# Performance work log

Hardware: AMD Instinct MI355X
Metric: run time of the kernel (lower is better)

Reference implementation:

```python
import jax, jax.numpy as jnp
import numpy as np

IMG_SIZE = 224  # matches init_kwargs img_size


def setup_inputs() -> dict:
    key = jax.random.key(0)
    k1, k2, k3 = jax.random.split(key, 3)
    B, N = 128, 16384
    points = jax.random.uniform(k1, (B, N, 3), dtype=jnp.float32, minval=-1.0, maxval=1.0)
    azimuth = jax.random.uniform(k2, (B,), dtype=jnp.float32, minval=0.0, maxval=2.0 * np.pi)
    elevation = jax.random.uniform(k3, (B,), dtype=jnp.float32, minval=-0.5, maxval=0.5)
    return {"points": points, "azimuth": azimuth, "elevation": elevation}


def _rotation_matrices(azimuth, elevation):
    cა, sა = jnp.cos(azimuth), jnp.sin(azimuth)
    ce, se = jnp.cos(elevation), jnp.sin(elevation)
    z = jnp.zeros_like(cა)
    o = jnp.ones_like(cა)
    # R_az: rotation about y-axis, shape (B,3,3)
    R_az = jnp.stack([
        jnp.stack([cა, z, sა], -1),
        jnp.stack([z, o, z], -1),
        jnp.stack([-sა, z, cა], -1),
    ], axis=-2)
    # R_el: rotation about x-axis
    R_el = jnp.stack([
        jnp.stack([o, z, z], -1),
        jnp.stack([z, ce, -se], -1),
        jnp.stack([z, se, ce], -1),
    ], axis=-2)
    return jnp.einsum('bij,bjk->bik', R_el, R_az)


def reference(points, azimuth, elevation):
    B, N, _ = points.shape
    H = W = IMG_SIZE
    R = _rotation_matrices(azimuth, elevation)                 # (B,3,3)
    rotated = jnp.einsum('bni,bji->bnj', points, R)            # points @ R^T -> (B,N,3)

    points_2d = rotated[..., :2]
    z = rotated[..., 2]
    z_min = jnp.min(z, axis=1, keepdims=True)
    z_max = jnp.max(z, axis=1, keepdims=True)
    feat = 0.3 + 0.7 * (z - z_min) / (z_max - z_min + 1e-6)    # (B,N)

    px = (points_2d[..., 0] + 1.0) * 0.5 * W - 0.5
    py = (points_2d[..., 1] + 1.0) * 0.5 * H - 0.5
    px1 = jnp.floor(px); py1 = jnp.floor(py)
    px2 = px1 + 1.0;     py2 = py1 + 1.0

    w11 = (px2 - px) * (py2 - py)
    w12 = (px2 - px) * (py - py1)
    w21 = (px - px1) * (py2 - py)
    w22 = (px - px1) * (py - py1)

    mask = (px1 >= 0) & (py1 >= 0) & (px2 < W) & (py2 < H)     # (B,N)
    # fuse mask + feature into the weights instead of compacting (jit-friendly)
    vals = jnp.stack([w11, w12, w21, w22], axis=-1)            # (B,N,4)
    vals = vals * (feat * mask.astype(feat.dtype))[..., None]

    px1i = jnp.clip(px1, 0, W - 1).astype(jnp.int32)
    py1i = jnp.clip(py1, 0, H - 1).astype(jnp.int32)
    px2i = jnp.clip(px2, 0, W - 1).astype(jnp.int32)
    py2i = jnp.clip(py2, 0, H - 1).astype(jnp.int32)
    base = (jnp.arange(B, dtype=jnp.int32) * (H * W))[:, None]  # (B,1)
    idx = jnp.stack([
        base + py1i * W + px1i,
        base + py2i * W + px1i,
        base + py1i * W + px2i,
        base + py2i * W + px2i,
    ], axis=-1)                                                 # (B,N,4)

    image = jnp.zeros(B * H * W, dtype=vals.dtype)
    image = image.at[idx.reshape(-1)].add(vals.reshape(-1))
    image = image.reshape(B, 1, H, W)
    return jnp.broadcast_to(image, (B, 3, H, W))
```

## Files before the change

kernel.cpp:

```cpp
#include <hip/hip_runtime.h>

#define IMG 224
#define HW (IMG * IMG)
#define HW4 (HW / 4)
#define NB 128
#define NPTS 16384

#define QUARTERS 4
#define RPB (IMG / QUARTERS)
#define TILE_FLOATS (RPB * IMG)
#define THREADS 512

__global__ __launch_bounds__(THREADS) void k_render(const float* __restrict__ pts,
                                                    const float* __restrict__ az,
                                                    const float* __restrict__ el,
                                                    float* __restrict__ out) {
    const int b = blockIdx.x & (NB - 1);
    const int q = blockIdx.x >> 7;
    const int y0 = q * RPB;

    __shared__ float tile[TILE_FLOATS];
    __shared__ float wmin[THREADS / 64], wmax[THREADS / 64];

    float sa, ca, se, ce;
    __sincosf(az[b], &sa, &ca);
    __sincosf(el[b], &se, &ce);
    const float r00 = ca,       r02 = sa;
    const float r10 = se * sa,  r11 = ce,  r12 = -se * ca;
    const float r20 = -ce * sa, r21 = se,  r22 = ce * ca;

    for (int i = threadIdx.x; i < TILE_FLOATS; i += THREADS) tile[i] = 0.0f;

    const float4* __restrict__ pb4 = (const float4*)(pts + (size_t)b * NPTS * 3);

    float zmin = 1e30f, zmax = -1e30f;
    for (int it = 0; it < NPTS / (4 * THREADS); ++it) {
        const int t = it * THREADS + threadIdx.x;
        const float4 v0 = pb4[3 * t + 0];
        const float4 v1 = pb4[3 * t + 1];
        const float4 v2 = pb4[3 * t + 2];
        float rz;
        rz = r20 * v0.x + r21 * v0.y + r22 * v0.z; zmin = fminf(zmin, rz); zmax = fmaxf(zmax, rz);
        rz = r20 * v0.w + r21 * v1.x + r22 * v1.y; zmin = fminf(zmin, rz); zmax = fmaxf(zmax, rz);
        rz = r20 * v1.z + r21 * v1.w + r22 * v2.x; zmin = fminf(zmin, rz); zmax = fmaxf(zmax, rz);
        rz = r20 * v2.y + r21 * v2.z + r22 * v2.w; zmin = fminf(zmin, rz); zmax = fmaxf(zmax, rz);
    }
    for (int m = 1; m < 64; m <<= 1) {
        zmin = fminf(zmin, __shfl_xor(zmin, m));
        zmax = fmaxf(zmax, __shfl_xor(zmax, m));
    }
    const int wid = threadIdx.x >> 6;
    if ((threadIdx.x & 63) == 0) { wmin[wid] = zmin; wmax[wid] = zmax; }
    __syncthreads();
    zmin = wmin[0]; zmax = wmax[0];
#pragma unroll
    for (int w = 1; w < THREADS / 64; ++w) {
        zmin = fminf(zmin, wmin[w]);
        zmax = fmaxf(zmax, wmax[w]);
    }
    const float inv = 0.7f / (zmax - zmin + 1e-6f);

    auto splat = [&](float x, float y, float z) {
        const float rx = r00 * x + r02 * z;
        const float ry = r10 * x + r11 * y + r12 * z;
        const float rz = r20 * x + r21 * y + r22 * z;
        const float feat = 0.3f + (rz - zmin) * inv;

        const float px = (rx + 1.0f) * (0.5f * IMG) - 0.5f;
        const float py = (ry + 1.0f) * (0.5f * IMG) - 0.5f;
        const float px1 = floorf(px);
        const float py1 = floorf(py);
        if (px1 >= 0.0f && py1 >= 0.0f && px1 < (float)(IMG - 1) && py1 < (float)(IMG - 1)) {
            const float wx2 = px - px1;
            const float wx1 = 1.0f - wx2;
            const float wy2 = py - py1;
            const float wy1 = 1.0f - wy2;

            const int ix = (int)px1;
            const int iy = (int)py1;
            const int r0 = iy - y0;
            const int r1 = r0 + 1;
            if (r0 >= 0 && r0 < RPB) {
                atomicAdd(&tile[r0 * IMG + ix],     wx1 * wy1 * feat);
                atomicAdd(&tile[r0 * IMG + ix + 1], wx2 * wy1 * feat);
            }
            if (r1 >= 0 && r1 < RPB) {
                atomicAdd(&tile[r1 * IMG + ix],     wx1 * wy2 * feat);
                atomicAdd(&tile[r1 * IMG + ix + 1], wx2 * wy2 * feat);
            }
        }
    };

    for (int it = 0; it < NPTS / (4 * THREADS); ++it) {
        const int t = it * THREADS + threadIdx.x;
        const float4 v0 = pb4[3 * t + 0];
        const float4 v1 = pb4[3 * t + 1];
        const float4 v2 = pb4[3 * t + 2];
        splat(v0.x, v0.y, v0.z);
        splat(v0.w, v1.x, v1.y);
        splat(v1.z, v1.w, v2.x);
        splat(v2.y, v2.z, v2.w);
    }

    __syncthreads();

    const float4* __restrict__ t4 = (const float4*)tile;
    float4* __restrict__ o4 = (float4*)(out + (size_t)b * 3 * HW + (size_t)y0 * IMG);
    for (int i = threadIdx.x; i < TILE_FLOATS / 4; i += THREADS) {
        const float4 v = t4[i];
        o4[i] = v;
        o4[i + HW4] = v;
        o4[i + 2 * HW4] = v;
    }
}

extern "C" void kernel_launch(void* const* d_in, const int* in_sizes, int n_in,
                              void* d_out, int out_size, void* d_ws, size_t ws_size,
                              hipStream_t stream) {
    const float* pts = (const float*)d_in[0];
    const float* az  = (const float*)d_in[1];
    const float* el  = (const float*)d_in[2];
    float* out = (float*)d_out;

    k_render<<<NB * QUARTERS, THREADS, 0, stream>>>(pts, az, el, out);
}
```

Before: 133.5 us.

## Split render into transform/min-max prep kernel and row-banded splat kernel

After: 148.0 us. 10.8% more time.

```diff
diff --git a/kernel.cpp b/kernel.cpp
--- a/kernel.cpp
+++ b/kernel.cpp
@@ -6,21 +6,26 @@
 #define NB 128
 #define NPTS 16384
 
-#define QUARTERS 4
-#define RPB (IMG / QUARTERS)
-#define TILE_FLOATS (RPB * IMG)
-#define THREADS 512
+#define PACKED_FLOATS ((size_t)NB * NPTS * 3)
+#define MINKEY_BYTE_OFF (PACKED_FLOATS * sizeof(float))
 
-__global__ __launch_bounds__(THREADS) void k_render(const float* __restrict__ pts,
-                                                    const float* __restrict__ az,
-                                                    const float* __restrict__ el,
-                                                    float* __restrict__ out) {
+__device__ __forceinline__ unsigned fkey(float f) {
+    unsigned u = __float_as_uint(f);
+    return (u & 0x80000000u) ? ~u : (u | 0x80000000u);
+}
+__device__ __forceinline__ float fdec(unsigned k) {
+    unsigned u = (k & 0x80000000u) ? (k & 0x7FFFFFFFu) : ~k;
+    return __uint_as_float(u);
+}
+
+__global__ __launch_bounds__(256) void k_prep(const float* __restrict__ pts,
+                                              const float* __restrict__ az,
+                                              const float* __restrict__ el,
+                                              float* __restrict__ packed,
+                                              unsigned* __restrict__ minkeys,
+                                              unsigned* __restrict__ maxkeys) {
     const int b = blockIdx.x & (NB - 1);
-    const int q = blockIdx.x >> 7;
-    const int y0 = q * RPB;
-
-    __shared__ float tile[TILE_FLOATS];
-    __shared__ float wmin[THREADS / 64], wmax[THREADS / 64];
+    const int chunk = blockIdx.x >> 7;
 
     float sa, ca, se, ce;
     __sincosf(az[b], &sa, &ca);
@@ -29,53 +34,85 @@
     const float r10 = se * sa,  r11 = ce,  r12 = -se * ca;
     const float r20 = -ce * sa, r21 = se,  r22 = ce * ca;
 
-    for (int i = threadIdx.x; i < TILE_FLOATS; i += THREADS) tile[i] = 0.0f;
-
     const float4* __restrict__ pb4 = (const float4*)(pts + (size_t)b * NPTS * 3);
+    float4* __restrict__ pk4 = (float4*)(packed + (size_t)b * NPTS * 3);
 
     float zmin = 1e30f, zmax = -1e30f;
-    for (int it = 0; it < NPTS / (4 * THREADS); ++it) {
-        const int t = it * THREADS + threadIdx.x;
+
+    auto xform = [&](float x, float y, float z, float& px, float& py, float& rz) {
+        const float rx = r00 * x + r02 * z;
+        const float ry = r10 * x + r11 * y + r12 * z;
+        rz = r20 * x + r21 * y + r22 * z;
+        px = (rx + 1.0f) * (0.5f * IMG) - 0.5f;
+        py = (ry + 1.0f) * (0.5f * IMG) - 0.5f;
+        zmin = fminf(zmin, rz);
+        zmax = fmaxf(zmax, rz);
+    };
+
+#pragma unroll
+    for (int it = 0; it < 2; ++it) {
+        const int t = chunk * 512 + it * 256 + threadIdx.x;
         const float4 v0 = pb4[3 * t + 0];
         const float4 v1 = pb4[3 * t + 1];
         const float4 v2 = pb4[3 * t + 2];
-        float rz;
-        rz = r20 * v0.x + r21 * v0.y + r22 * v0.z; zmin = fminf(zmin, rz); zmax = fmaxf(zmax, rz);
-        rz = r20 * v0.w + r21 * v1.x + r22 * v1.y; zmin = fminf(zmin, rz); zmax = fmaxf(zmax, rz);
-        rz = r20 * v1.z + r21 * v1.w + r22 * v2.x; zmin = fminf(zmin, rz); zmax = fmaxf(zmax, rz);
-        rz = r20 * v2.y + r21 * v2.z + r22 * v2.w; zmin = fminf(zmin, rz); zmax = fmaxf(zmax, rz);
+        float px0, py0, rz0, px1, py1, rz1, px2, py2, rz2, px3, py3, rz3;
+        xform(v0.x, v0.y, v0.z, px0, py0, rz0);
+        xform(v0.w, v1.x, v1.y, px1, py1, rz1);
+        xform(v1.z, v1.w, v2.x, px2, py2, rz2);
+        xform(v2.y, v2.z, v2.w, px3, py3, rz3);
+        pk4[3 * t + 0] = make_float4(px0, py0, rz0, px1);
+        pk4[3 * t + 1] = make_float4(py1, rz1, px2, py2);
+        pk4[3 * t + 2] = make_float4(rz2, px3, py3, rz3);
     }
+
     for (int m = 1; m < 64; m <<= 1) {
         zmin = fminf(zmin, __shfl_xor(zmin, m));
         zmax = fmaxf(zmax, __shfl_xor(zmax, m));
     }
+    __shared__ float wmin[4], wmax[4];
     const int wid = threadIdx.x >> 6;
     if ((threadIdx.x & 63) == 0) { wmin[wid] = zmin; wmax[wid] = zmax; }
     __syncthreads();
-    zmin = wmin[0]; zmax = wmax[0];
-#pragma unroll
-    for (int w = 1; w < THREADS / 64; ++w) {
-        zmin = fminf(zmin, wmin[w]);
-        zmax = fmaxf(zmax, wmax[w]);
+    if (threadIdx.x == 0) {
+        zmin = fminf(fminf(wmin[0], wmin[1]), fminf(wmin[2], wmin[3]));
+        zmax = fmaxf(fmaxf(wmax[0], wmax[1]), fmaxf(wmax[2], wmax[3]));
+        atomicMin(&minkeys[b], fkey(zmin));
+        atomicMax(&maxkeys[b], fkey(zmax));
     }
+}
+
+#define GROUPS 8
+#define RPB (IMG / GROUPS)
+#define TILE_FLOATS (RPB * IMG)
+#define BTHREADS 512
+
+__global__ __launch_bounds__(BTHREADS) void k_splat(const float* __restrict__ packed,
+                                                    const unsigned* __restrict__ minkeys,
+                                                    const unsigned* __restrict__ maxkeys,
+                                                    float* __restrict__ out) {
+    const int b = blockIdx.x & (NB - 1);
+    const int g = blockIdx.x >> 7;
+    const int y0 = g * RPB;
+
+    __shared__ float tile[TILE_FLOATS];
+    for (int i = threadIdx.x; i < TILE_FLOATS; i += BTHREADS) tile[i] = 0.0f;
+
+    const float zmin = fdec(minkeys[b]);
+    const float zmax = fdec(maxkeys[b]);
     const float inv = 0.7f / (zmax - zmin + 1e-6f);
+    __syncthreads();
 
-    auto splat = [&](float x, float y, float z) {
-        const float rx = r00 * x + r02 * z;
-        const float ry = r10 * x + r11 * y + r12 * z;
-        const float rz = r20 * x + r21 * y + r22 * z;
-        const float feat = 0.3f + (rz - zmin) * inv;
+    const float4* __restrict__ pk4 = (const float4*)(packed + (size_t)b * NPTS * 3);
 
-        const float px = (rx + 1.0f) * (0.5f * IMG) - 0.5f;
-        const float py = (ry + 1.0f) * (0.5f * IMG) - 0.5f;
+    auto splat = [&](float px, float py, float rz) {
         const float px1 = floorf(px);
         const float py1 = floorf(py);
         if (px1 >= 0.0f && py1 >= 0.0f && px1 < (float)(IMG - 1) && py1 < (float)(IMG - 1)) {
+            const float feat = 0.3f + (rz - zmin) * inv;
             const float wx2 = px - px1;
             const float wx1 = 1.0f - wx2;
             const float wy2 = py - py1;
             const float wy1 = 1.0f - wy2;
-
             const int ix = (int)px1;
             const int iy = (int)py1;
             const int r0 = iy - y0;
@@ -91,22 +128,23 @@
         }
     };
 
-    for (int it = 0; it < NPTS / (4 * THREADS); ++it) {
-        const int t = it * THREADS + threadIdx.x;
-        const float4 v0 = pb4[3 * t + 0];
-        const float4 v1 = pb4[3 * t + 1];
-        const float4 v2 = pb4[3 * t + 2];
-        splat(v0.x, v0.y, v0.z);
-        splat(v0.w, v1.x, v1.y);
-        splat(v1.z, v1.w, v2.x);
-        splat(v2.y, v2.z, v2.w);
+#pragma unroll
+    for (int it = 0; it < NPTS / 4 / BTHREADS; ++it) {
+        const int t = it * BTHREADS + threadIdx.x;
+        const float4 w0 = pk4[3 * t + 0];
+        const float4 w1 = pk4[3 * t + 1];
+        const float4 w2 = pk4[3 * t + 2];
+        splat(w0.x, w0.y, w0.z);
+        splat(w0.w, w1.x, w1.y);
+        splat(w1.z, w1.w, w2.x);
+        splat(w2.y, w2.z, w2.w);
     }
 
     __syncthreads();
 
     const float4* __restrict__ t4 = (const float4*)tile;
     float4* __restrict__ o4 = (float4*)(out + (size_t)b * 3 * HW + (size_t)y0 * IMG);
-    for (int i = threadIdx.x; i < TILE_FLOATS / 4; i += THREADS) {
+    for (int i = threadIdx.x; i < TILE_FLOATS / 4; i += BTHREADS) {
         const float4 v = t4[i];
         o4[i] = v;
         o4[i + HW4] = v;
@@ -122,5 +160,13 @@
     const float* el  = (const float*)d_in[2];
     float* out = (float*)d_out;
 
-    k_render<<<NB * QUARTERS, THREADS, 0, stream>>>(pts, az, el, out);
+    float* packed = (float*)d_ws;
+    unsigned* minkeys = (unsigned*)((char*)d_ws + MINKEY_BYTE_OFF);
+    unsigned* maxkeys = minkeys + NB;
+
+    hipMemsetAsync(minkeys, 0xFF, NB * sizeof(unsigned), stream);
+    hipMemsetAsync(maxkeys, 0x00, NB * sizeof(unsigned), stream);
+
+    k_prep<<<NB * 8, 256, 0, stream>>>(pts, az, el, packed, minkeys, maxkeys);
+    k_splat<<<NB * GROUPS, BTHREADS, 0, stream>>>(packed, minkeys, maxkeys, out);
 }
```

## Split image into halves with 1024-thread blocks and cache rotated points in registers

Applied to the files above, without the earlier changes.

New measurement: 134.4 us. No clear change (+0.7%).

```diff
diff --git a/kernel.cpp b/kernel.cpp
--- a/kernel.cpp
+++ b/kernel.cpp
@@ -6,21 +6,25 @@
 #define NB 128
 #define NPTS 16384
 
-#define QUARTERS 4
-#define RPB (IMG / QUARTERS)
-#define TILE_FLOATS (RPB * IMG)
-#define THREADS 512
+#define THREADS 1024
+#define HALF_ROWS 112
+#define TILE_FLOATS (HALF_ROWS * IMG)
+#define PPT (NPTS / THREADS)
+#define NWAVES (THREADS / 64)
+#define SMEM_FLOATS (TILE_FLOATS + 2 * NWAVES)
 
 __global__ __launch_bounds__(THREADS) void k_render(const float* __restrict__ pts,
                                                     const float* __restrict__ az,
                                                     const float* __restrict__ el,
                                                     float* __restrict__ out) {
+    extern __shared__ float smem[];
+    float* tile = smem;
+    float* wmin = smem + TILE_FLOATS;
+    float* wmax = wmin + NWAVES;
+
     const int b = blockIdx.x & (NB - 1);
-    const int q = blockIdx.x >> 7;
-    const int y0 = q * RPB;
-
-    __shared__ float tile[TILE_FLOATS];
-    __shared__ float wmin[THREADS / 64], wmax[THREADS / 64];
+    const int h = blockIdx.x >> 7;
+    const int y0 = h * HALF_ROWS;
 
     float sa, ca, se, ce;
     __sincosf(az[b], &sa, &ca);
@@ -29,77 +33,73 @@
     const float r10 = se * sa,  r11 = ce,  r12 = -se * ca;
     const float r20 = -ce * sa, r21 = se,  r22 = ce * ca;
 
-    for (int i = threadIdx.x; i < TILE_FLOATS; i += THREADS) tile[i] = 0.0f;
-
     const float4* __restrict__ pb4 = (const float4*)(pts + (size_t)b * NPTS * 3);
 
+    float px[PPT], py[PPT], rz[PPT];
     float zmin = 1e30f, zmax = -1e30f;
-    for (int it = 0; it < NPTS / (4 * THREADS); ++it) {
+
+#pragma unroll
+    for (int it = 0; it < PPT / 4; ++it) {
         const int t = it * THREADS + threadIdx.x;
         const float4 v0 = pb4[3 * t + 0];
         const float4 v1 = pb4[3 * t + 1];
         const float4 v2 = pb4[3 * t + 2];
-        float rz;
-        rz = r20 * v0.x + r21 * v0.y + r22 * v0.z; zmin = fminf(zmin, rz); zmax = fmaxf(zmax, rz);
-        rz = r20 * v0.w + r21 * v1.x + r22 * v1.y; zmin = fminf(zmin, rz); zmax = fmaxf(zmax, rz);
-        rz = r20 * v1.z + r21 * v1.w + r22 * v2.x; zmin = fminf(zmin, rz); zmax = fmaxf(zmax, rz);
-        rz = r20 * v2.y + r21 * v2.z + r22 * v2.w; zmin = fminf(zmin, rz); zmax = fmaxf(zmax, rz);
+        const float xs[4] = {v0.x, v0.w, v1.z, v2.y};
+        const float ys[4] = {v0.y, v1.x, v1.w, v2.z};
+        const float zs[4] = {v0.z, v1.y, v2.x, v2.w};
+#pragma unroll
+        for (int j = 0; j < 4; ++j) {
+            const int k = it * 4 + j;
+            const float x = xs[j], y = ys[j], z = zs[j];
+            const float rx = r00 * x + r02 * z;
+            const float ry = r10 * x + r11 * y + r12 * z;
+            const float zz = r20 * x + r21 * y + r22 * z;
+            px[k] = (rx + 1.0f) * (0.5f * IMG) - 0.5f;
+            py[k] = (ry + 1.0f) * (0.5f * IMG) - 0.5f;
+            rz[k] = zz;
+            zmin = fminf(zmin, zz);
+            zmax = fmaxf(zmax, zz);
+        }
     }
+
     for (int m = 1; m < 64; m <<= 1) {
         zmin = fminf(zmin, __shfl_xor(zmin, m));
         zmax = fmaxf(zmax, __shfl_xor(zmax, m));
     }
     const int wid = threadIdx.x >> 6;
     if ((threadIdx.x & 63) == 0) { wmin[wid] = zmin; wmax[wid] = zmax; }
+
+    for (int i = threadIdx.x; i < TILE_FLOATS; i += THREADS) tile[i] = 0.0f;
     __syncthreads();
-    zmin = wmin[0]; zmax = wmax[0];
+
 #pragma unroll
-    for (int w = 1; w < THREADS / 64; ++w) {
+    for (int w = 0; w < NWAVES; ++w) {
         zmin = fminf(zmin, wmin[w]);
         zmax = fmaxf(zmax, wmax[w]);
     }
     const float inv = 0.7f / (zmax - zmin + 1e-6f);
 
-    auto splat = [&](float x, float y, float z) {
-        const float rx = r00 * x + r02 * z;
-        const float ry = r10 * x + r11 * y + r12 * z;
-        const float rz = r20 * x + r21 * y + r22 * z;
-        const float feat = 0.3f + (rz - zmin) * inv;
-
-        const float px = (rx + 1.0f) * (0.5f * IMG) - 0.5f;
-        const float py = (ry + 1.0f) * (0.5f * IMG) - 0.5f;
-        const float px1 = floorf(px);
-        const float py1 = floorf(py);
-        if (px1 >= 0.0f && py1 >= 0.0f && px1 < (float)(IMG - 1) && py1 < (float)(IMG - 1)) {
-            const float wx2 = px - px1;
-            const float wx1 = 1.0f - wx2;
-            const float wy2 = py - py1;
-            const float wy1 = 1.0f - wy2;
-
-            const int ix = (int)px1;
-            const int iy = (int)py1;
-            const int r0 = iy - y0;
+#pragma unroll
+    for (int k = 0; k < PPT; ++k) {
+        const float p = px[k], q = py[k];
+        const float fx1 = floorf(p);
+        const float fy1 = floorf(q);
+        if (fx1 >= 0.0f && fy1 >= 0.0f && fx1 < (float)(IMG - 1) && fy1 < (float)(IMG - 1)) {
+            const float feat = 0.3f + (rz[k] - zmin) * inv;
+            const float wx2 = p - fx1, wx1 = 1.0f - wx2;
+            const float wy2 = q - fy1, wy1 = 1.0f - wy2;
+            const int ix = (int)fx1;
+            const int r0 = (int)fy1 - y0;
             const int r1 = r0 + 1;
-            if (r0 >= 0 && r0 < RPB) {
+            if (r0 >= 0 && r0 < HALF_ROWS) {
                 atomicAdd(&tile[r0 * IMG + ix],     wx1 * wy1 * feat);
                 atomicAdd(&tile[r0 * IMG + ix + 1], wx2 * wy1 * feat);
             }
-            if (r1 >= 0 && r1 < RPB) {
+            if (r1 >= 0 && r1 < HALF_ROWS) {
                 atomicAdd(&tile[r1 * IMG + ix],     wx1 * wy2 * feat);
                 atomicAdd(&tile[r1 * IMG + ix + 1], wx2 * wy2 * feat);
             }
         }
-    };
-
-    for (int it = 0; it < NPTS / (4 * THREADS); ++it) {
-        const int t = it * THREADS + threadIdx.x;
-        const float4 v0 = pb4[3 * t + 0];
-        const float4 v1 = pb4[3 * t + 1];
-        const float4 v2 = pb4[3 * t + 2];
-        splat(v0.x, v0.y, v0.z);
-        splat(v0.w, v1.x, v1.y);
-        splat(v1.z, v1.w, v2.x);
-        splat(v2.y, v2.z, v2.w);
     }
 
     __syncthreads();
@@ -122,5 +122,5 @@
     const float* el  = (const float*)d_in[2];
     float* out = (float*)d_out;
 
-    k_render<<<NB * QUARTERS, THREADS, 0, stream>>>(pts, az, el, out);
+    k_render<<<NB * 2, THREADS, SMEM_FLOATS * sizeof(float), stream>>>(pts, az, el, out);
 }
```

## Split z-range reduction into separate kernel and double-buffer point loads into LDS

Applied to the files above, without the earlier changes.

After: 143.6 us. +7.6%, slower.

```diff
diff --git a/kernel.cpp b/kernel.cpp
--- a/kernel.cpp
+++ b/kernel.cpp
@@ -6,36 +6,24 @@
 #define NB 128
 #define NPTS 16384
 
-#define QUARTERS 4
-#define RPB (IMG / QUARTERS)
-#define TILE_FLOATS (RPB * IMG)
-#define THREADS 512
-
-__global__ __launch_bounds__(THREADS) void k_render(const float* __restrict__ pts,
-                                                    const float* __restrict__ az,
-                                                    const float* __restrict__ el,
-                                                    float* __restrict__ out) {
-    const int b = blockIdx.x & (NB - 1);
-    const int q = blockIdx.x >> 7;
-    const int y0 = q * RPB;
-
-    __shared__ float tile[TILE_FLOATS];
-    __shared__ float wmin[THREADS / 64], wmax[THREADS / 64];
+__global__ __launch_bounds__(1024) void k_minmax(const float* __restrict__ pts,
+                                                 const float* __restrict__ az,
+                                                 const float* __restrict__ el,
+                                                 float* __restrict__ params) {
+    const int b = blockIdx.x;
+    const int tid = threadIdx.x;
 
     float sa, ca, se, ce;
     __sincosf(az[b], &sa, &ca);
     __sincosf(el[b], &se, &ce);
-    const float r00 = ca,       r02 = sa;
-    const float r10 = se * sa,  r11 = ce,  r12 = -se * ca;
-    const float r20 = -ce * sa, r21 = se,  r22 = ce * ca;
-
-    for (int i = threadIdx.x; i < TILE_FLOATS; i += THREADS) tile[i] = 0.0f;
+    const float r20 = -ce * sa, r21 = se, r22 = ce * ca;
 
     const float4* __restrict__ pb4 = (const float4*)(pts + (size_t)b * NPTS * 3);
 
     float zmin = 1e30f, zmax = -1e30f;
-    for (int it = 0; it < NPTS / (4 * THREADS); ++it) {
-        const int t = it * THREADS + threadIdx.x;
+#pragma unroll
+    for (int it = 0; it < 4; ++it) {
+        const int t = it * 1024 + tid;
         const float4 v0 = pb4[3 * t + 0];
         const float4 v1 = pb4[3 * t + 1];
         const float4 v2 = pb4[3 * t + 2];
@@ -45,68 +33,131 @@
         rz = r20 * v1.z + r21 * v1.w + r22 * v2.x; zmin = fminf(zmin, rz); zmax = fmaxf(zmax, rz);
         rz = r20 * v2.y + r21 * v2.z + r22 * v2.w; zmin = fminf(zmin, rz); zmax = fmaxf(zmax, rz);
     }
+
     for (int m = 1; m < 64; m <<= 1) {
         zmin = fminf(zmin, __shfl_xor(zmin, m));
         zmax = fmaxf(zmax, __shfl_xor(zmax, m));
     }
-    const int wid = threadIdx.x >> 6;
-    if ((threadIdx.x & 63) == 0) { wmin[wid] = zmin; wmax[wid] = zmax; }
+    __shared__ float wmin[16], wmax[16];
+    const int wid = tid >> 6;
+    if ((tid & 63) == 0) { wmin[wid] = zmin; wmax[wid] = zmax; }
     __syncthreads();
-    zmin = wmin[0]; zmax = wmax[0];
+    if (tid == 0) {
 #pragma unroll
-    for (int w = 1; w < THREADS / 64; ++w) {
-        zmin = fminf(zmin, wmin[w]);
-        zmax = fmaxf(zmax, wmax[w]);
+        for (int w = 1; w < 16; ++w) {
+            zmin = fminf(zmin, wmin[w]);
+            zmax = fmaxf(zmax, wmax[w]);
+        }
+        params[2 * b + 0] = zmin;
+        params[2 * b + 1] = 0.7f / (zmax - zmin + 1e-6f);
     }
-    const float inv = 0.7f / (zmax - zmin + 1e-6f);
+}
 
-    auto splat = [&](float x, float y, float z) {
+#define SROWS 56
+#define TILEF (SROWS * IMG)
+#define CH_PTS 1024
+#define CH_FLOATS (CH_PTS * 3)
+#define NCH (NPTS / CH_PTS)
+
+__global__ __launch_bounds__(512) void k_splat(const float* __restrict__ pts,
+                                               const float* __restrict__ az,
+                                               const float* __restrict__ el,
+                                               const float* __restrict__ params,
+                                               float* __restrict__ out) {
+    __shared__ __align__(16) float tile[TILEF];
+    __shared__ __align__(16) float buf[2][CH_FLOATS];
+
+    const int b = blockIdx.x & (NB - 1);
+    const int q = blockIdx.x >> 7;
+    const int y0 = q * SROWS;
+    const int tid = threadIdx.x;
+    const int w = tid >> 6;
+    const int l = tid & 63;
+
+    float sa, ca, se, ce;
+    __sincosf(az[b], &sa, &ca);
+    __sincosf(el[b], &se, &ce);
+    const float r00 = ca,       r02 = sa;
+    const float r10 = se * sa,  r11 = ce,  r12 = -se * ca;
+    const float r20 = -ce * sa, r21 = se,  r22 = ce * ca;
+
+    const float zmin = params[2 * b + 0];
+    const float inv  = params[2 * b + 1];
+    asm volatile("" :: "v"(zmin), "v"(inv));
+
+    for (int i = tid; i < TILEF; i += 512) tile[i] = 0.0f;
+
+    const char* gbase = (const char*)(pts + (size_t)b * NPTS * 3);
+
+    auto stage = [&](int c, int bi) {
+        const char* g = gbase + (size_t)c * 12288;
+        char* lb = (char*)buf[bi];
+        __builtin_amdgcn_global_load_lds(
+            (const __attribute__((address_space(1))) void*)(g + (w * 64 + l) * 16),
+            (__attribute__((address_space(3))) void*)(lb + w * 1024), 16, 0, 0);
+        if (w < 4) {
+            __builtin_amdgcn_global_load_lds(
+                (const __attribute__((address_space(1))) void*)(g + 8192 + (w * 64 + l) * 16),
+                (__attribute__((address_space(3))) void*)(lb + 8192 + w * 1024), 16, 0, 0);
+        }
+    };
+
+    auto proc = [&](float x, float y, float z) {
         const float rx = r00 * x + r02 * z;
         const float ry = r10 * x + r11 * y + r12 * z;
         const float rz = r20 * x + r21 * y + r22 * z;
-        const float feat = 0.3f + (rz - zmin) * inv;
-
         const float px = (rx + 1.0f) * (0.5f * IMG) - 0.5f;
         const float py = (ry + 1.0f) * (0.5f * IMG) - 0.5f;
-        const float px1 = floorf(px);
-        const float py1 = floorf(py);
-        if (px1 >= 0.0f && py1 >= 0.0f && px1 < (float)(IMG - 1) && py1 < (float)(IMG - 1)) {
-            const float wx2 = px - px1;
-            const float wx1 = 1.0f - wx2;
-            const float wy2 = py - py1;
-            const float wy1 = 1.0f - wy2;
-
-            const int ix = (int)px1;
-            const int iy = (int)py1;
-            const int r0 = iy - y0;
+        const float fx = floorf(px);
+        const float fy = floorf(py);
+        if (fx >= 0.0f && fy >= 0.0f && fx < (float)(IMG - 1) && fy < (float)(IMG - 1)) {
+            const float feat = 0.3f + (rz - zmin) * inv;
+            const float wx2 = px - fx, wx1 = 1.0f - wx2;
+            const float wy2 = py - fy, wy1 = 1.0f - wy2;
+            const int ix = (int)fx;
+            const int r0 = (int)fy - y0;
             const int r1 = r0 + 1;
-            if (r0 >= 0 && r0 < RPB) {
+            if (r0 >= 0 && r0 < SROWS) {
                 atomicAdd(&tile[r0 * IMG + ix],     wx1 * wy1 * feat);
                 atomicAdd(&tile[r0 * IMG + ix + 1], wx2 * wy1 * feat);
             }
-            if (r1 >= 0 && r1 < RPB) {
+            if (r1 >= 0 && r1 < SROWS) {
                 atomicAdd(&tile[r1 * IMG + ix],     wx1 * wy2 * feat);
                 atomicAdd(&tile[r1 * IMG + ix + 1], wx2 * wy2 * feat);
             }
         }
     };
 
-    for (int it = 0; it < NPTS / (4 * THREADS); ++it) {
-        const int t = it * THREADS + threadIdx.x;
-        const float4 v0 = pb4[3 * t + 0];
-        const float4 v1 = pb4[3 * t + 1];
-        const float4 v2 = pb4[3 * t + 2];
-        splat(v0.x, v0.y, v0.z);
-        splat(v0.w, v1.x, v1.y);
-        splat(v1.z, v1.w, v2.x);
-        splat(v2.y, v2.z, v2.w);
+    stage(0, 0);
+    stage(1, 1);
+    asm volatile("s_waitcnt lgkmcnt(0)" ::: "memory");
+
+    for (int i = 0; i < NCH; ++i) {
+        if (i < NCH - 1) {
+            if (w < 4) asm volatile("s_waitcnt vmcnt(2)" ::: "memory");
+            else       asm volatile("s_waitcnt vmcnt(1)" ::: "memory");
+        } else {
+            asm volatile("s_waitcnt vmcnt(0)" ::: "memory");
+        }
+        __builtin_amdgcn_s_barrier();
+
+        const float2* c2 = (const float2*)buf[i & 1];
+        const float2 a0 = c2[3 * tid + 0];
+        const float2 a1 = c2[3 * tid + 1];
+        const float2 a2 = c2[3 * tid + 2];
+        proc(a0.x, a0.y, a1.x);
+        proc(a1.y, a2.x, a2.y);
+
+        __builtin_amdgcn_s_barrier();
+        if (i + 2 < NCH) stage(i + 2, i & 1);
     }
 
-    __syncthreads();
+    asm volatile("s_waitcnt lgkmcnt(0)" ::: "memory");
+    __builtin_amdgcn_s_barrier();
 
     const float4* __restrict__ t4 = (const float4*)tile;
     float4* __restrict__ o4 = (float4*)(out + (size_t)b * 3 * HW + (size_t)y0 * IMG);
-    for (int i = threadIdx.x; i < TILE_FLOATS / 4; i += THREADS) {
+    for (int i = tid; i < TILEF / 4; i += 512) {
         const float4 v = t4[i];
         o4[i] = v;
         o4[i + HW4] = v;
@@ -120,7 +171,9 @@
     const float* pts = (const float*)d_in[0];
     const float* az  = (const float*)d_in[1];
     const float* el  = (const float*)d_in[2];
+    float* params = (float*)d_ws;
     float* out = (float*)d_out;
 
-    k_render<<<NB * QUARTERS, THREADS, 0, stream>>>(pts, az, el, out);
+    k_minmax<<<NB, 1024, 0, stream>>>(pts, az, el, params);
+    k_splat<<<NB * 4, 512, 0, stream>>>(pts, az, el, params, out);
 }
```
